# Performance work log

Hardware: AMD Instinct MI355X
Metric: run time of the kernel (lower is better)

## Reference

```python
import jax, jax.numpy as jnp
import numpy as np

B, I, H1, H2, E, T = 16384, 512, 256, 128, 8, 2


def setup_inputs() -> dict:
    key = jax.random.key(0)
    ks = jax.random.split(key, 4)
    # Xavier-ish scaling for stability
    x = jax.random.normal(ks[0], (B, I), dtype=jnp.float32)
    W1 = jax.random.normal(ks[1], (E, I, H1), dtype=jnp.float32) / np.sqrt(I)
    b1 = jnp.zeros((E, H1), dtype=jnp.float32)
    W2 = jax.random.normal(ks[2], (E, H1, H2), dtype=jnp.float32) / np.sqrt(H1)
    b2 = jnp.zeros((E, H2), dtype=jnp.float32)
    Wg = jax.random.normal(ks[3], (T, I, E), dtype=jnp.float32) / np.sqrt(I)
    bg = jnp.zeros((T, E), dtype=jnp.float32)
    return {"x": x, "W1": W1, "b1": b1, "W2": W2, "b2": b2, "Wg": Wg, "bg": bg}


def reference(x, W1, b1, W2, b2, Wg, bg):
    # All experts as one grouped GEMM: [E, B, H1]
    h = jax.nn.relu(jnp.einsum('bi,eih->ebh', x, W1) + b1[:, None, :])
    # Last expert layer (lastlayer_reg=True -> act applied): [E, B, H2]
    e_out = jax.nn.relu(jnp.einsum('ebh,eho->ebo', h, W2) + b2[:, None, :])
    # Per-task gates with softmax over experts: [T, B, E]
    gates = jax.nn.softmax(jnp.einsum('bi,tie->tbe', x, Wg) + bg[:, None, :], axis=-1)
    # Gate-weighted combine of expert outputs: [T, B, H2]
    towers = jnp.einsum('tbe,ebo->tbo', gates, e_out)
    return towers
```

## Files before the change

### kernel.cpp

```cpp
#include <hip/hip_runtime.h>
#include <hip/hip_bf16.h>

#define B_  16384
#define I_  512
#define H1_ 256
#define H2_ 128
#define E_  8
#define T_  2

typedef __attribute__((ext_vector_type(8))) short short8;
typedef __attribute__((ext_vector_type(4))) float float4_t;

__device__ inline unsigned short f2bf(float f) {
    union { float f; unsigned u; } v; v.f = f;
    unsigned r = v.u + 0x7FFFu + ((v.u >> 16) & 1u);
    return (unsigned short)(r >> 16);
}

__device__ inline void async_copy16(const unsigned short* g, unsigned short* l) {
    __builtin_amdgcn_global_load_lds(
        (const __attribute__((address_space(1))) void*)g,
        (__attribute__((address_space(3))) void*)l,
        16, 0, 0);
}

__global__ void transpose_bf16_kernel(const float* __restrict__ in, unsigned short* __restrict__ out,
                                      int R, int C) {
    __shared__ float tile[32][33];
    int e = blockIdx.z;
    int c0 = blockIdx.x * 32;
    int r0 = blockIdx.y * 32;
    const float* inp = in + (size_t)e * R * C;
    unsigned short* outp = out + (size_t)e * R * C;
    int tx = threadIdx.x, ty = threadIdx.y;
#pragma unroll
    for (int j = 0; j < 32; j += 8)
        tile[ty + j][tx] = inp[(size_t)(r0 + ty + j) * C + c0 + tx];
    __syncthreads();
#pragma unroll
    for (int j = 0; j < 32; j += 8)
        outp[(size_t)(c0 + ty + j) * R + r0 + tx] = f2bf(tile[tx][ty + j]);
}

__global__ void prep_wgt_kernel(const float* __restrict__ wg, unsigned short* __restrict__ wgt) {
    int idx = blockIdx.x * 256 + threadIdx.x;
    int te = idx >> 9;
    int i  = idx & 511;
    int t = te >> 3, e = te & 7;
    wgt[(size_t)te * I_ + i] = f2bf(wg[(size_t)t * I_ * E_ + (size_t)i * E_ + e]);
}

__global__ void gates_conv_kernel(const float* __restrict__ x,
                                  unsigned short* __restrict__ xb,
                                  const unsigned short* __restrict__ wgt,
                                  const float* __restrict__ bg,
                                  float* __restrict__ gates) {
    int w = threadIdx.x >> 6, lane = threadIdx.x & 63;
    int row0 = (blockIdx.x * 4 + w) * 16;
    int col = lane & 15, quad = lane >> 4;
    float4_t acc = {0.f, 0.f, 0.f, 0.f};
    const float* xr = x + (size_t)(row0 + col) * I_ + quad * 8;
    unsigned short* xbr = xb + (size_t)(row0 + col) * I_ + quad * 8;
    const unsigned short* bG = wgt + (size_t)col * I_ + quad * 8;
#pragma unroll
    for (int k = 0; k < I_; k += 32) {
        float4_t xa = *(const float4_t*)(xr + k);
        float4_t xc = *(const float4_t*)(xr + k + 4);
        short8 a;
        a[0] = (short)f2bf(xa[0]); a[1] = (short)f2bf(xa[1]);
        a[2] = (short)f2bf(xa[2]); a[3] = (short)f2bf(xa[3]);
        a[4] = (short)f2bf(xc[0]); a[5] = (short)f2bf(xc[1]);
        a[6] = (short)f2bf(xc[2]); a[7] = (short)f2bf(xc[3]);
        *(short8*)(xbr + k) = a;
        short8 b = *(const short8*)(bG + k);
        acc = __builtin_amdgcn_mfma_f32_16x16x32_bf16(a, b, acc, 0, 0, 0);
    }
    float bias = bg[col];
#pragma unroll
    for (int p = 0; p < 4; ++p) {
        float v = acc[p] + bias;
        float m = v;
        m = fmaxf(m, __shfl_xor(m, 1));
        m = fmaxf(m, __shfl_xor(m, 2));
        m = fmaxf(m, __shfl_xor(m, 4));
        float ev = __expf(v - m);
        float s = ev;
        s += __shfl_xor(s, 1);
        s += __shfl_xor(s, 2);
        s += __shfl_xor(s, 4);
        gates[(size_t)col * B_ + row0 + quad * 4 + p] = ev / s;
    }
}

__global__ void gemm_relu_kernel(const unsigned short* __restrict__ A, size_t aSE,
                                 const unsigned short* __restrict__ Bt, size_t bSE,
                                 const float* __restrict__ bias, int biasSE,
                                 unsigned short* __restrict__ C, size_t cSE,
                                 int K, int lda, int ldb, int ldc) {
    __shared__ unsigned short As[128 * 64];
    __shared__ unsigned short Bs[128 * 64];
    int e = blockIdx.z;
    const unsigned short* Ae = A + (size_t)e * aSE;
    const unsigned short* Be = Bt + (size_t)e * bSE;
    const float* biasE = bias + (size_t)e * biasSE;
    unsigned short* Ce = C + (size_t)e * cSE;
    int m0 = blockIdx.x * 128, n0 = blockIdx.y * 128;
    int t = threadIdx.x, w = t >> 6, lane = t & 63;
    int col = lane & 15, quad = lane >> 4;
    int wm = (w & 1) * 64, wn = (w >> 1) * 64;

    float4_t acc[4][4];
#pragma unroll
    for (int mi = 0; mi < 4; ++mi)
#pragma unroll
        for (int ni = 0; ni < 4; ++ni)
            acc[mi][ni] = (float4_t){0.f, 0.f, 0.f, 0.f};

    int rT = t >> 3;
    int gk = (((t & 7) ^ (rT & 7))) * 8;
    const unsigned short* aG = Ae + (size_t)(m0 + rT) * lda + gk;
    const unsigned short* bG = Be + (size_t)(n0 + rT) * ldb + gk;
    unsigned short* aL = As + (size_t)w * 64 * 8;
    unsigned short* bL = Bs + (size_t)w * 64 * 8;

    for (int k0 = 0; k0 < K; k0 += 64) {
#pragma unroll
        for (int j = 0; j < 4; ++j) {
            async_copy16(aG + (size_t)j * 32 * lda + k0, aL + j * 2048);
            async_copy16(bG + (size_t)j * 32 * ldb + k0, bL + j * 2048);
        }
        __syncthreads();
#pragma unroll
        for (int kk = 0; kk < 64; kk += 32) {
            int q = (kk >> 3) + quad;
            short8 af[4], bf[4];
#pragma unroll
            for (int mi = 0; mi < 4; ++mi) {
                int r = wm + mi * 16 + col;
                af[mi] = *(const short8*)&As[r * 64 + ((q ^ (r & 7)) * 8)];
            }
#pragma unroll
            for (int ni = 0; ni < 4; ++ni) {
                int r = wn + ni * 16 + col;
                bf[ni] = *(const short8*)&Bs[r * 64 + ((q ^ (r & 7)) * 8)];
            }
#pragma unroll
            for (int mi = 0; mi < 4; ++mi)
#pragma unroll
                for (int ni = 0; ni < 4; ++ni)
                    acc[mi][ni] = __builtin_amdgcn_mfma_f32_16x16x32_bf16(af[mi], bf[ni], acc[mi][ni], 0, 0, 0);
        }
        __syncthreads();
    }

#pragma unroll
    for (int ni = 0; ni < 4; ++ni) {
        int c = n0 + wn + ni * 16 + col;
        float bv = biasE[c];
#pragma unroll
        for (int mi = 0; mi < 4; ++mi) {
            int rbase = m0 + wm + mi * 16 + quad * 4;
#pragma unroll
            for (int p = 0; p < 4; ++p) {
                float v = acc[mi][ni][p] + bv;
                v = v > 0.f ? v : 0.f;
                Ce[(size_t)(rbase + p) * ldc + c] = f2bf(v);
            }
        }
    }
}

__global__ void fused_l2_combine_kernel(const unsigned short* __restrict__ h,
                                        const unsigned short* __restrict__ w2t,
                                        const float* __restrict__ b2,
                                        const float* __restrict__ gates,
                                        float* __restrict__ out) {
    __shared__ unsigned short As[32 * 128];
    __shared__ unsigned short Bs[128 * 128];
    __shared__ float gL[16 * 32];

    int b0 = blockIdx.x * 32;
    int t = threadIdx.x, w = t >> 6, lane = t & 63;
    int col = lane & 15, quad = lane >> 4;
    int wn = w * 32;

    if (t < 128) {
        int te = t >> 3, i4 = (t & 7) * 4;
        *(float4_t*)&gL[te * 32 + i4] = *(const float4_t*)&gates[(size_t)te * B_ + b0 + i4];
    }

    float4_t tw0[2][2], tw1[2][2];
#pragma unroll
    for (int mi = 0; mi < 2; ++mi)
#pragma unroll
        for (int ni = 0; ni < 2; ++ni) {
            tw0[mi][ni] = (float4_t){0.f, 0.f, 0.f, 0.f};
            tw1[mi][ni] = (float4_t){0.f, 0.f, 0.f, 0.f};
        }

    int rT = t >> 4;
    int slot = t & 15;

    for (int e = 0; e < E_; ++e) {
        const unsigned short* hE = h + (size_t)e * B_ * H1_;
        const unsigned short* w2E = w2t + (size_t)e * H2_ * H1_;

        float4_t acc[2][2];
#pragma unroll
        for (int mi = 0; mi < 2; ++mi)
#pragma unroll
            for (int ni = 0; ni < 2; ++ni)
                acc[mi][ni] = (float4_t){0.f, 0.f, 0.f, 0.f};

        for (int k0 = 0; k0 < H1_; k0 += 128) {
#pragma unroll
            for (int j = 0; j < 2; ++j) {
                int row = j * 16 + rT;
                int gk = (((slot ^ row) & 7) | (slot & 8)) * 8;
                async_copy16(hE + (size_t)(b0 + row) * H1_ + k0 + gk,
                             As + j * 2048 + w * 512);
            }
#pragma unroll
            for (int j = 0; j < 8; ++j) {
                int row = j * 16 + rT;
                int gk = (((slot ^ row) & 7) | (slot & 8)) * 8;
                async_copy16(w2E + (size_t)row * H1_ + k0 + gk,
                             Bs + j * 2048 + w * 512);
            }
            __syncthreads();
#pragma unroll
            for (int kk = 0; kk < 128; kk += 32) {
                int q = (kk >> 3) + quad;
                short8 af[2], bfr[2];
#pragma unroll
                for (int mi = 0; mi < 2; ++mi) {
                    int r = mi * 16 + col;
                    int sw = ((q & 8) | ((q ^ r) & 7)) * 8;
                    af[mi] = *(const short8*)&As[r * 128 + sw];
                }
#pragma unroll
                for (int ni = 0; ni < 2; ++ni) {
                    int r = wn + ni * 16 + col;
                    int sw = ((q & 8) | ((q ^ r) & 7)) * 8;
                    bfr[ni] = *(const short8*)&Bs[r * 128 + sw];
                }
#pragma unroll
                for (int mi = 0; mi < 2; ++mi)
#pragma unroll
                    for (int ni = 0; ni < 2; ++ni)
                        acc[mi][ni] = __builtin_amdgcn_mfma_f32_16x16x32_bf16(af[mi], bfr[ni], acc[mi][ni], 0, 0, 0);
            }
            __syncthreads();
        }

#pragma unroll
        for (int mi = 0; mi < 2; ++mi) {
            float4_t g0 = *(const float4_t*)&gL[e * 32 + mi * 16 + quad * 4];
            float4_t g1 = *(const float4_t*)&gL[(8 + e) * 32 + mi * 16 + quad * 4];
#pragma unroll
            for (int ni = 0; ni < 2; ++ni) {
                float bv = b2[e * H2_ + wn + ni * 16 + col];
#pragma unroll
                for (int p = 0; p < 4; ++p) {
                    float v = acc[mi][ni][p] + bv;
                    v = v > 0.f ? v : 0.f;
                    tw0[mi][ni][p] += g0[p] * v;
                    tw1[mi][ni][p] += g1[p] * v;
                }
            }
        }
    }

#pragma unroll
    for (int mi = 0; mi < 2; ++mi) {
#pragma unroll
        for (int ni = 0; ni < 2; ++ni) {
            int n = wn + ni * 16 + col;
#pragma unroll
            for (int p = 0; p < 4; ++p) {
                int r = b0 + mi * 16 + quad * 4 + p;
                out[(size_t)r * H2_ + n] = tw0[mi][ni][p];
                out[(size_t)B_ * H2_ + (size_t)r * H2_ + n] = tw1[mi][ni][p];
            }
        }
    }
}

extern "C" void kernel_launch(void* const* d_in, const int* in_sizes, int n_in,
                              void* d_out, int out_size, void* d_ws, size_t ws_size,
                              hipStream_t stream) {
    const float* x  = (const float*)d_in[0];
    const float* W1 = (const float*)d_in[1];
    const float* b1 = (const float*)d_in[2];
    const float* W2 = (const float*)d_in[3];
    const float* b2 = (const float*)d_in[4];
    const float* Wg = (const float*)d_in[5];
    const float* bg = (const float*)d_in[6];
    float* out = (float*)d_out;

    char* ws = (char*)d_ws;
    unsigned short* xb    = (unsigned short*)(ws);
    unsigned short* w1t   = (unsigned short*)(ws + 16777216);
    unsigned short* w2t   = (unsigned short*)(ws + 18874368);
    unsigned short* wgt   = (unsigned short*)(ws + 19398656);
    float*          gates = (float*)(ws + 19415040);
    unsigned short* h     = (unsigned short*)(ws + 20463616);

    transpose_bf16_kernel<<<dim3(H1_ / 32, I_ / 32, E_), dim3(32, 8), 0, stream>>>(W1, w1t, I_, H1_);
    transpose_bf16_kernel<<<dim3(H2_ / 32, H1_ / 32, E_), dim3(32, 8), 0, stream>>>(W2, w2t, H1_, H2_);
    prep_wgt_kernel<<<dim3(T_ * E_ * I_ / 256), 256, 0, stream>>>(Wg, wgt);

    gates_conv_kernel<<<dim3(B_ / 64), 256, 0, stream>>>(x, xb, wgt, bg, gates);

    gemm_relu_kernel<<<dim3(B_ / 128, H1_ / 128, E_), 256, 0, stream>>>(
        xb, 0, w1t, (size_t)H1_ * I_, b1, H1_, h, (size_t)B_ * H1_, I_, I_, I_, H1_);

    fused_l2_combine_kernel<<<dim3(B_ / 32), 256, 0, stream>>>(h, w2t, b2, gates, out);
}
```

Measured before the change: 172.9 us.

## Split gate K across waves, stage GEMM epilogue in LDS, split combine over N

The gate kernel now splits the K dimension across four waves per 16-row block and reduces the partials through shared memory, which gives four times as many blocks. The layer-1 GEMM epilogue now writes bf16 results into shared memory first and then stores them as coalesced 16-byte rows, replacing scattered 2-byte global stores. The fused layer-2/combine kernel is split into two halves of the output columns, doubling the grid and halving each block's W2 tile and accumulators. In exchange, the h tile is re-read by both column halves, and the epilogue gains an extra synchronisation.

```diff
diff --git a/kernel.cpp b/kernel.cpp
--- a/kernel.cpp
+++ b/kernel.cpp
@@ -50,46 +50,49 @@
     wgt[(size_t)te * I_ + i] = f2bf(wg[(size_t)t * I_ * E_ + (size_t)i * E_ + e]);
 }
 
-__global__ void gates_conv_kernel(const float* __restrict__ x,
-                                  unsigned short* __restrict__ xb,
-                                  const unsigned short* __restrict__ wgt,
-                                  const float* __restrict__ bg,
-                                  float* __restrict__ gates) {
-    int w = threadIdx.x >> 6, lane = threadIdx.x & 63;
-    int row0 = (blockIdx.x * 4 + w) * 16;
+__global__ void gates_split_kernel(const float* __restrict__ x,
+                                   unsigned short* __restrict__ xb,
+                                   const unsigned short* __restrict__ wgt,
+                                   const float* __restrict__ bg,
+                                   float* __restrict__ gates) {
+    __shared__ float red[4][16][16];
+    int t = threadIdx.x, w = t >> 6, lane = t & 63;
     int col = lane & 15, quad = lane >> 4;
+    int b0 = blockIdx.x * 16;
+    int k0 = w * 128;
+    const float* xr = x + (size_t)(b0 + col) * I_ + k0 + quad * 8;
+    unsigned short* xw = xb + (size_t)(b0 + col) * I_ + k0 + quad * 8;
+    const unsigned short* bGp = wgt + (size_t)col * I_ + k0 + quad * 8;
     float4_t acc = {0.f, 0.f, 0.f, 0.f};
-    const float* xr = x + (size_t)(row0 + col) * I_ + quad * 8;
-    unsigned short* xbr = xb + (size_t)(row0 + col) * I_ + quad * 8;
-    const unsigned short* bG = wgt + (size_t)col * I_ + quad * 8;
-#pragma unroll
-    for (int k = 0; k < I_; k += 32) {
-        float4_t xa = *(const float4_t*)(xr + k);
-        float4_t xc = *(const float4_t*)(xr + k + 4);
+#pragma unroll
+    for (int ks = 0; ks < 128; ks += 32) {
+        float4_t xa = *(const float4_t*)(xr + ks);
+        float4_t xc = *(const float4_t*)(xr + ks + 4);
         short8 a;
         a[0] = (short)f2bf(xa[0]); a[1] = (short)f2bf(xa[1]);
         a[2] = (short)f2bf(xa[2]); a[3] = (short)f2bf(xa[3]);
         a[4] = (short)f2bf(xc[0]); a[5] = (short)f2bf(xc[1]);
         a[6] = (short)f2bf(xc[2]); a[7] = (short)f2bf(xc[3]);
-        *(short8*)(xbr + k) = a;
-        short8 b = *(const short8*)(bG + k);
+        *(short8*)(xw + ks) = a;
+        short8 b = *(const short8*)(bGp + ks);
         acc = __builtin_amdgcn_mfma_f32_16x16x32_bf16(a, b, acc, 0, 0, 0);
     }
-    float bias = bg[col];
-#pragma unroll
-    for (int p = 0; p < 4; ++p) {
-        float v = acc[p] + bias;
-        float m = v;
-        m = fmaxf(m, __shfl_xor(m, 1));
-        m = fmaxf(m, __shfl_xor(m, 2));
-        m = fmaxf(m, __shfl_xor(m, 4));
-        float ev = __expf(v - m);
-        float s = ev;
-        s += __shfl_xor(s, 1);
-        s += __shfl_xor(s, 2);
-        s += __shfl_xor(s, 4);
-        gates[(size_t)col * B_ + row0 + quad * 4 + p] = ev / s;
-    }
+#pragma unroll
+    for (int p = 0; p < 4; ++p)
+        red[w][quad * 4 + p][col] = acc[p];
+    __syncthreads();
+    int r = t >> 4, te = t & 15;
+    float v = red[0][r][te] + red[1][r][te] + red[2][r][te] + red[3][r][te] + bg[te];
+    float m = v;
+    m = fmaxf(m, __shfl_xor(m, 1));
+    m = fmaxf(m, __shfl_xor(m, 2));
+    m = fmaxf(m, __shfl_xor(m, 4));
+    float ev = __expf(v - m);
+    float s = ev;
+    s += __shfl_xor(s, 1);
+    s += __shfl_xor(s, 2);
+    s += __shfl_xor(s, 4);
+    gates[(size_t)te * B_ + b0 + r] = ev / s;
 }
 
 __global__ void gemm_relu_kernel(const unsigned short* __restrict__ A, size_t aSE,
@@ -97,8 +100,9 @@
                                  const float* __restrict__ bias, int biasSE,
                                  unsigned short* __restrict__ C, size_t cSE,
                                  int K, int lda, int ldb, int ldc) {
-    __shared__ unsigned short As[128 * 64];
-    __shared__ unsigned short Bs[128 * 64];
+    __shared__ unsigned short smem[128 * 128];
+    unsigned short* As = smem;
+    unsigned short* Bs = smem + 128 * 64;
     int e = blockIdx.z;
     const unsigned short* Ae = A + (size_t)e * aSE;
     const unsigned short* Be = Bt + (size_t)e * bSE;
@@ -152,21 +156,29 @@
         }
         __syncthreads();
     }
-
+    unsigned short* Ct = smem;
 #pragma unroll
     for (int ni = 0; ni < 4; ++ni) {
-        int c = n0 + wn + ni * 16 + col;
-        float bv = biasE[c];
+        int c = wn + ni * 16 + col;
+        float bv = biasE[n0 + c];
 #pragma unroll
         for (int mi = 0; mi < 4; ++mi) {
-            int rbase = m0 + wm + mi * 16 + quad * 4;
+            int rbase = wm + mi * 16 + quad * 4;
 #pragma unroll
             for (int p = 0; p < 4; ++p) {
                 float v = acc[mi][ni][p] + bv;
                 v = v > 0.f ? v : 0.f;
-                Ce[(size_t)(rbase + p) * ldc + c] = f2bf(v);
-            }
-        }
+                Ct[(rbase + p) * 128 + c] = f2bf(v);
+            }
+        }
+    }
+    __syncthreads();
+    int rr = t >> 4, sl = t & 15;
+#pragma unroll
+    for (int pass = 0; pass < 8; ++pass) {
+        int row = pass * 16 + rr;
+        short8 vv = *(const short8*)&Ct[row * 128 + sl * 8];
+        *(short8*)&Ce[(size_t)(m0 + row) * ldc + n0 + sl * 8] = vv;
     }
 }
 
@@ -176,41 +188,38 @@
                                         const float* __restrict__ gates,
                                         float* __restrict__ out) {
     __shared__ unsigned short As[32 * 128];
-    __shared__ unsigned short Bs[128 * 128];
+    __shared__ unsigned short Bs[64 * 128];
     __shared__ float gL[16 * 32];
 
     int b0 = blockIdx.x * 32;
+    int nh = blockIdx.y * 64;
     int t = threadIdx.x, w = t >> 6, lane = t & 63;
     int col = lane & 15, quad = lane >> 4;
-    int wn = w * 32;
+    int wn = w * 16;
 
     if (t < 128) {
         int te = t >> 3, i4 = (t & 7) * 4;
         *(float4_t*)&gL[te * 32 + i4] = *(const float4_t*)&gates[(size_t)te * B_ + b0 + i4];
     }
 
-    float4_t tw0[2][2], tw1[2][2];
-#pragma unroll
-    for (int mi = 0; mi < 2; ++mi)
-#pragma unroll
-        for (int ni = 0; ni < 2; ++ni) {
-            tw0[mi][ni] = (float4_t){0.f, 0.f, 0.f, 0.f};
-            tw1[mi][ni] = (float4_t){0.f, 0.f, 0.f, 0.f};
-        }
+    float4_t tw0[2], tw1[2];
+#pragma unroll
+    for (int mi = 0; mi < 2; ++mi) {
+        tw0[mi] = (float4_t){0.f, 0.f, 0.f, 0.f};
+        tw1[mi] = (float4_t){0.f, 0.f, 0.f, 0.f};
+    }
 
     int rT = t >> 4;
     int slot = t & 15;
 
     for (int e = 0; e < E_; ++e) {
         const unsigned short* hE = h + (size_t)e * B_ * H1_;
-        const unsigned short* w2E = w2t + (size_t)e * H2_ * H1_;
-
-        float4_t acc[2][2];
+        const unsigned short* w2E = w2t + (size_t)e * H2_ * H1_ + (size_t)nh * H1_;
+
+        float4_t acc[2];
 #pragma unroll
         for (int mi = 0; mi < 2; ++mi)
-#pragma unroll
-            for (int ni = 0; ni < 2; ++ni)
-                acc[mi][ni] = (float4_t){0.f, 0.f, 0.f, 0.f};
+            acc[mi] = (float4_t){0.f, 0.f, 0.f, 0.f};
 
         for (int k0 = 0; k0 < H1_; k0 += 128) {
 #pragma unroll
@@ -221,7 +230,7 @@
                              As + j * 2048 + w * 512);
             }
 #pragma unroll
-            for (int j = 0; j < 8; ++j) {
+            for (int j = 0; j < 4; ++j) {
                 int row = j * 16 + rT;
                 int gk = (((slot ^ row) & 7) | (slot & 8)) * 8;
                 async_copy16(w2E + (size_t)row * H1_ + k0 + gk,
@@ -231,57 +240,48 @@
 #pragma unroll
             for (int kk = 0; kk < 128; kk += 32) {
                 int q = (kk >> 3) + quad;
-                short8 af[2], bfr[2];
+                short8 af[2], bfr;
 #pragma unroll
                 for (int mi = 0; mi < 2; ++mi) {
                     int r = mi * 16 + col;
                     int sw = ((q & 8) | ((q ^ r) & 7)) * 8;
                     af[mi] = *(const short8*)&As[r * 128 + sw];
                 }
-#pragma unroll
-                for (int ni = 0; ni < 2; ++ni) {
-                    int r = wn + ni * 16 + col;
+                {
+                    int r = wn + col;
                     int sw = ((q & 8) | ((q ^ r) & 7)) * 8;
-                    bfr[ni] = *(const short8*)&Bs[r * 128 + sw];
+                    bfr = *(const short8*)&Bs[r * 128 + sw];
                 }
 #pragma unroll
                 for (int mi = 0; mi < 2; ++mi)
-#pragma unroll
-                    for (int ni = 0; ni < 2; ++ni)
-                        acc[mi][ni] = __builtin_amdgcn_mfma_f32_16x16x32_bf16(af[mi], bfr[ni], acc[mi][ni], 0, 0, 0);
+                    acc[mi] = __builtin_amdgcn_mfma_f32_16x16x32_bf16(af[mi], bfr, acc[mi], 0, 0, 0);
             }
             __syncthreads();
         }
 
+        float bv = b2[e * H2_ + nh + wn + col];
 #pragma unroll
         for (int mi = 0; mi < 2; ++mi) {
             float4_t g0 = *(const float4_t*)&gL[e * 32 + mi * 16 + quad * 4];
             float4_t g1 = *(const float4_t*)&gL[(8 + e) * 32 + mi * 16 + quad * 4];
 #pragma unroll
-            for (int ni = 0; ni < 2; ++ni) {
-                float bv = b2[e * H2_ + wn + ni * 16 + col];
-#pragma unroll
-                for (int p = 0; p < 4; ++p) {
-                    float v = acc[mi][ni][p] + bv;
-                    v = v > 0.f ? v : 0.f;
-                    tw0[mi][ni][p] += g0[p] * v;
-                    tw1[mi][ni][p] += g1[p] * v;
-                }
-            }
-        }
-    }
-
+            for (int p = 0; p < 4; ++p) {
+                float v = acc[mi][p] + bv;
+                v = v > 0.f ? v : 0.f;
+                tw0[mi][p] += g0[p] * v;
+                tw1[mi][p] += g1[p] * v;
+            }
+        }
+    }
+
+    int n = nh + wn + col;
 #pragma unroll
     for (int mi = 0; mi < 2; ++mi) {
 #pragma unroll
-        for (int ni = 0; ni < 2; ++ni) {
-            int n = wn + ni * 16 + col;
-#pragma unroll
-            for (int p = 0; p < 4; ++p) {
-                int r = b0 + mi * 16 + quad * 4 + p;
-                out[(size_t)r * H2_ + n] = tw0[mi][ni][p];
-                out[(size_t)B_ * H2_ + (size_t)r * H2_ + n] = tw1[mi][ni][p];
-            }
+        for (int p = 0; p < 4; ++p) {
+            int r = b0 + mi * 16 + quad * 4 + p;
+            out[(size_t)r * H2_ + n] = tw0[mi][p];
+            out[(size_t)B_ * H2_ + (size_t)r * H2_ + n] = tw1[mi][p];
         }
     }
 }
@@ -310,10 +310,10 @@
     transpose_bf16_kernel<<<dim3(H2_ / 32, H1_ / 32, E_), dim3(32, 8), 0, stream>>>(W2, w2t, H1_, H2_);
     prep_wgt_kernel<<<dim3(T_ * E_ * I_ / 256), 256, 0, stream>>>(Wg, wgt);
 
-    gates_conv_kernel<<<dim3(B_ / 64), 256, 0, stream>>>(x, xb, wgt, bg, gates);
+    gates_split_kernel<<<dim3(B_ / 16), 256, 0, stream>>>(x, xb, wgt, bg, gates);
 
     gemm_relu_kernel<<<dim3(B_ / 128, H1_ / 128, E_), 256, 0, stream>>>(
         xb, 0, w1t, (size_t)H1_ * I_, b1, H1_, h, (size_t)B_ * H1_, I_, I_, I_, H1_);
 
-    fused_l2_combine_kernel<<<dim3(B_ / 32), 256, 0, stream>>>(h, w2t, b2, gates, out);
-}
+    fused_l2_combine_kernel<<<dim3(B_ / 32, 2), 256, 0, stream>>>(h, w2t, b2, gates, out);
+}
```

Measured after the change: 165.1 us. 1.05x faster.
